# Kernel optimization log

Measured on AMD Instinct MI355X. Metric: run time of the kernel, lower is better.

The kernel has to match this reference:

```python
import jax, jax.numpy as jnp
import numpy as np

GROUP_SIZE = 128


def dequantize_int4(packed, scales, group_size=GROUP_SIZE, dtype=jnp.float16):
    # packed: [O, I//2] bytes; low nibble -> even cols, high nibble -> odd cols
    O = packed.shape[0]
    I = packed.shape[1] * 2
    low = (packed & 15).astype(jnp.int8) - 8
    high = ((packed >> 4) & 15).astype(jnp.int8) - 8
    unpacked = jnp.stack([low, high], axis=-1).reshape(O, I)  # interleave low/high
    G = I // group_size
    grouped = unpacked.reshape(O, G, group_size).astype(jnp.float32)
    deq = grouped * scales.astype(jnp.float32)[:, :, None]  # per-group scale
    return deq.reshape(O, I).astype(dtype)


def setup_inputs() -> dict:
    key = jax.random.key(0)
    k1, k2, k3 = jax.random.split(key, 3)
    B, S, IN, OUT = 4, 2048, 4096, 11008
    G = IN // GROUP_SIZE
    x = jax.random.normal(k1, (B, S, IN), dtype=jnp.float16)
    packed = jax.random.randint(k2, (OUT, IN // 2), 0, 256, dtype=jnp.int32)
    scales = (jax.random.uniform(k3, (OUT, G), dtype=jnp.float32) * 0.05 + 0.001).astype(jnp.float16)
    return {"x": x, "packed": packed, "scales": scales}


def reference(x, packed, scales):
    x = x.astype(jnp.float16)
    W = dequantize_int4(packed, scales)  # [OUT, IN] fp16
    # nn.functional.linear: x @ W^T
    return jnp.einsum('bsi,oi->bso', x, W)
```

## Files before the change

### kernel.cpp

```cpp
#include <hip/hip_runtime.h>

#define M_DIM 8192
#define N_DIM 11008
#define K_DIM 4096
#define GROUPS 32
#define WQROW 512
#define LDSK 72

typedef short s16x8 __attribute__((ext_vector_type(8)));
typedef _Float16 f16x8 __attribute__((ext_vector_type(8)));
typedef _Float16 h2 __attribute__((ext_vector_type(2)));
typedef float f32x4 __attribute__((ext_vector_type(4)));
typedef unsigned short u16;
typedef unsigned int u32;

union f32u { float f; unsigned u; };
union h16u { u16 u; _Float16 h; };

__device__ __forceinline__ u16 f2bf(float f) {
  f32u v; v.f = f;
  unsigned r = v.u + 0x7FFFu + ((v.u >> 16) & 1u);
  return (u16)(r >> 16);
}
__device__ __forceinline__ float bf2f(u16 b) {
  f32u v; v.u = ((unsigned)b) << 16; return v.f;
}
__device__ __forceinline__ float h2f(u16 b) {
  h16u v; v.u = b; return (float)v.h;
}

__global__ void probe_mode_kernel(const void* __restrict__ scales,
                                  int* __restrict__ mode_out) {
  __shared__ int cnt[3];
  int t = threadIdx.x;
  if (t < 3) cnt[t] = 0;
  __syncthreads();
  float f0 = ((const float*)scales)[t];
  u16  hu  = ((const u16*)scales)[t];
  float f1 = h2f(hu);
  float f2 = bf2f(hu);
  if (f0 > 0.0004f && f0 < 0.065f) atomicAdd(&cnt[0], 1);
  if (f1 > 0.0004f && f1 < 0.065f) atomicAdd(&cnt[1], 1);
  if (f2 > 0.0004f && f2 < 0.065f) atomicAdd(&cnt[2], 1);
  __syncthreads();
  if (t == 0) {
    int m;
    if      (cnt[1] >= 240) m = 1;
    else if (cnt[2] >= 240) m = 2;
    else                    m = 0;
    mode_out[0] = m;
  }
}

__global__ __launch_bounds__(256) void convert_x_nat_kernel(
    const float* __restrict__ xf, u16* __restrict__ xh,
    const int* __restrict__ modep) {
  if (modep && modep[0] != 0) return;
  const int total8 = M_DIM * (K_DIM / 8);
  int idx = blockIdx.x * 256 + threadIdx.x;
  const int stride = gridDim.x * 256;
  for (; idx < total8; idx += stride) {
    const float4* p = (const float4*)(xf + (size_t)idx * 8);
    float4 a = p[0], b = p[1];
    union { _Float16 h[8]; s16x8 v; } r;
    r.h[0] = (_Float16)a.x; r.h[1] = (_Float16)a.y;
    r.h[2] = (_Float16)a.z; r.h[3] = (_Float16)a.w;
    r.h[4] = (_Float16)b.x; r.h[5] = (_Float16)b.y;
    r.h[6] = (_Float16)b.z; r.h[7] = (_Float16)b.w;
    *(s16x8*)(xh + (size_t)idx * 8) = r.v;
  }
}

__global__ __launch_bounds__(256) void dequant_w_kernel(
    const int* __restrict__ packed, const float* __restrict__ scf,
    u16* __restrict__ wf, const int* __restrict__ modep) {
  if (modep && modep[0] != 0) return;
  const int total = N_DIM * (K_DIM / 8);
  int idx = blockIdx.x * 256 + threadIdx.x;
  const int stride = gridDim.x * 256;
  for (; idx < total; idx += stride) {
    const int col = idx >> 9;
    const int d   = idx & 511;
    const float s = scf[col * GROUPS + (d >> 4)];
    const int4 p  = ((const int4*)packed)[idx];
    const int vals[4] = {p.x, p.y, p.z, p.w};
    union { _Float16 h[8]; s16x8 v; } r;
    #pragma unroll
    for (int e = 0; e < 4; ++e) {
      int b = vals[e] & 255;
      r.h[2 * e]     = (_Float16)((float)((b & 15) - 8) * s);
      r.h[2 * e + 1] = (_Float16)((float)(((b >> 4) & 15) - 8) * s);
    }
    *(s16x8*)(wf + (size_t)idx * 8) = r.v;
  }
}

__global__ __launch_bounds__(256, 2) void q4gemm_big_kernel(
    const u16* __restrict__ xh,
    const u16* __restrict__ wf,
    float* __restrict__ out,
    const int* __restrict__ modep)
{
  if (modep && modep[0] != 0) return;

  __shared__ _Float16 As[4][128 * 64];

  const int tid  = threadIdx.x;
  const int lane = tid & 63;
  const int wv   = tid >> 6;
  const int wn   = wv * 64;
  const int ln15 = lane & 15;
  const int lk   = lane >> 4;

  int bid = blockIdx.x;
  int f   = (bid & 7) * 344 + (bid >> 3);
  int bn  = f / 64;
  int bm  = f - bn * 64;
  const int m0 = bm * 128;
  const int n0 = bn * 256;

  const u16* abase[4];
  #pragma unroll
  for (int q = 0; q < 4; ++q) {
    int row = q * 32 + wv * 8 + (lane >> 3);
    abase[q] = xh + (size_t)(m0 + row) * K_DIM + (((lane & 7) ^ (lane >> 3)) * 8);
  }

#define STAGE(PB, T) do { \
    _Float16* dst = &As[(PB)][0]; \
    _Pragma("unroll") \
    for (int q = 0; q < 4; ++q) \
      __builtin_amdgcn_global_load_lds( \
          (const __attribute__((address_space(1))) void*)(abase[q] + (T) * 64), \
          (__attribute__((address_space(3))) void*)(dst + q * 2048 + wv * 512), \
          16, 0, 0); \
  } while (0)

  const u16* pB[4];
  #pragma unroll
  for (int j = 0; j < 4; ++j) {
    int col = n0 + wn + j * 16 + ln15;
    pB[j] = wf + (size_t)col * K_DIM + lk * 8;
  }

#define LOADB(RB, T) do { \
    _Pragma("unroll") \
    for (int j = 0; j < 4; ++j) { \
      RB[j]     = *(const f16x8*)(pB[j] + (T) * 64); \
      RB[j + 4] = *(const f16x8*)(pB[j] + (T) * 64 + 32); \
    } \
  } while (0)

#define COMPUTE(RB, PB) do { \
    const _Float16* asb = &As[(PB)][0]; \
    _Pragma("unroll") \
    for (int kkc = 0; kkc < 2; ++kkc) { \
      _Pragma("unroll") \
      for (int i = 0; i < 8; ++i) { \
        const int row  = i * 16 + ln15; \
        const int slot = (kkc * 4 + lk) ^ (ln15 & 7); \
        f16x8 af = *(const f16x8*)&asb[row * 64 + slot * 8]; \
        acc[i][0] = __builtin_amdgcn_mfma_f32_16x16x32_f16(af, RB[kkc * 4 + 0], acc[i][0], 0, 0, 0); \
        acc[i][1] = __builtin_amdgcn_mfma_f32_16x16x32_f16(af, RB[kkc * 4 + 1], acc[i][1], 0, 0, 0); \
        acc[i][2] = __builtin_amdgcn_mfma_f32_16x16x32_f16(af, RB[kkc * 4 + 2], acc[i][2], 0, 0, 0); \
        acc[i][3] = __builtin_amdgcn_mfma_f32_16x16x32_f16(af, RB[kkc * 4 + 3], acc[i][3], 0, 0, 0); \
      } \
    } \
  } while (0)

  f32x4 acc[8][4];
  #pragma unroll
  for (int i = 0; i < 8; ++i)
    #pragma unroll
    for (int j = 0; j < 4; ++j)
      acc[i][j] = f32x4{0.f, 0.f, 0.f, 0.f};

  f16x8 rbE[8], rbO[8];

  STAGE(0, 0);
  STAGE(1, 1);
  STAGE(2, 2);
  STAGE(3, 3);
  LOADB(rbE, 0);
  LOADB(rbO, 1);
  asm volatile("s_waitcnt vmcnt(0)" ::: "memory");
  __builtin_amdgcn_s_barrier();

  #pragma unroll 1
  for (int P = 0; P < 32; ++P) {
    const int b0 = (P & 1) * 2;
    const int s0 = b0 ^ 2;

    if (P > 0) {
      asm volatile("s_waitcnt vmcnt(16)" ::: "memory");
      __builtin_amdgcn_s_barrier();
      __builtin_amdgcn_sched_barrier(0);
      if (P <= 30) {
        STAGE(s0, 2 * P + 2);
        STAGE(s0 + 1, 2 * P + 3);
      }
      __builtin_amdgcn_sched_barrier(0);
    }

    const int tE = (2 * P + 2 > 63) ? 63 : (2 * P + 2);
    const int tO = (2 * P + 3 > 63) ? 63 : (2 * P + 3);

    __builtin_amdgcn_s_setprio(1);
    COMPUTE(rbE, b0);
    __builtin_amdgcn_s_setprio(0);
    LOADB(rbE, tE);

    __builtin_amdgcn_s_setprio(1);
    COMPUTE(rbO, b0 + 1);
    __builtin_amdgcn_s_setprio(0);
    LOADB(rbO, tO);
  }

  #pragma unroll
  for (int i = 0; i < 8; ++i) {
    int r0 = m0 + i * 16 + (lane >> 4) * 4;
    #pragma unroll
    for (int j = 0; j < 4; ++j) {
      int cc = n0 + wn + j * 16 + ln15;
      #pragma unroll
      for (int r = 0; r < 4; ++r)
        __builtin_nontemporal_store(acc[i][j][r], &out[(size_t)(r0 + r) * N_DIM + cc]);
    }
  }
#undef STAGE
#undef LOADB
#undef COMPUTE
}

__global__ __launch_bounds__(256) void convert_x_perm_kernel(
    const float* __restrict__ xf, u16* __restrict__ xh,
    const int* __restrict__ modep) {
  if (modep && modep[0] != 0) return;
  const int total8 = M_DIM * (K_DIM / 8);
  int idx = blockIdx.x * 256 + threadIdx.x;
  const int stride = gridDim.x * 256;
  for (; idx < total8; idx += stride) {
    const float4* p = (const float4*)(xf + (size_t)idx * 8);
    float4 a = p[0], b = p[1];
    union { _Float16 h[8]; s16x8 v; } r;
    r.h[0] = (_Float16)a.x; r.h[1] = (_Float16)b.x;
    r.h[2] = (_Float16)a.y; r.h[3] = (_Float16)b.y;
    r.h[4] = (_Float16)a.z; r.h[5] = (_Float16)b.z;
    r.h[6] = (_Float16)a.w; r.h[7] = (_Float16)b.w;
    *(s16x8*)(xh + (size_t)idx * 8) = r.v;
  }
}

__global__ __launch_bounds__(256) void repack_w_kernel(
    const int* __restrict__ packed, u32* __restrict__ wq) {
  const int total = N_DIM * WQROW;
  int idx = blockIdx.x * 256 + threadIdx.x;
  const int stride = gridDim.x * 256;
  for (; idx < total; idx += stride) {
    const int4 p = ((const int4*)packed)[idx];
    wq[idx] = (u32)(p.x & 255) | ((u32)(p.y & 255) << 8) |
              ((u32)(p.z & 255) << 16) | ((u32)p.w << 24);
  }
}

__device__ __forceinline__ f16x8 dq8(u32 q, h2 s2) {
  const u32 M = 0x000F000Fu, G = 0x64006400u;
  const h2 bias = {(_Float16)(-1032.0f), (_Float16)(-1032.0f)};
  union { u32 u; h2 h; } a0, a1, a2, a3;
  a0.u = (q & M) | G;
  a1.u = ((q >> 4) & M) | G;
  a2.u = ((q >> 8) & M) | G;
  a3.u = ((q >> 12) & M) | G;
  a0.h = (a0.h + bias) * s2;
  a1.h = (a1.h + bias) * s2;
  a2.h = (a2.h + bias) * s2;
  a3.h = (a3.h + bias) * s2;
  union { u32 u[4]; f16x8 f; } r;
  r.u[0] = a0.u; r.u[1] = a1.u; r.u[2] = a2.u; r.u[3] = a3.u;
  return r.f;
}

__global__ __launch_bounds__(256, 2) void q4gemm_mid_kernel(
    const u16* __restrict__ xh, const u32* __restrict__ wq,
    const float* __restrict__ scf, float* __restrict__ out,
    const int* __restrict__ modep)
{
  if (modep && modep[0] != 0) return;

  __shared__ _Float16 As[3][128 * 64];

  const int tid  = threadIdx.x;
  const int lane = tid & 63;
  const int wv   = tid >> 6;
  const int wn   = wv * 64;
  const int ln15 = lane & 15;
  const int lk   = lane >> 4;

  int bid = blockIdx.x;
  int f   = (bid & 7) * 344 + (bid >> 3);
  int bn  = f / 64;
  int bm  = f - bn * 64;
  const int m0 = bm * 128;
  const int n0 = bn * 256;

  const u16* abase[4];
  #pragma unroll
  for (int q = 0; q < 4; ++q) {
    int row = q * 32 + wv * 8 + (lane >> 3);
    abase[q] = xh + (size_t)(m0 + row) * K_DIM + (((lane & 7) ^ (lane >> 3)) * 8);
  }

#define STAGE(PB, T) do { \
    _Float16* dst = &As[(PB)][0]; \
    _Pragma("unroll") \
    for (int q = 0; q < 4; ++q) \
      __builtin_amdgcn_global_load_lds( \
          (const __attribute__((address_space(1))) void*)(abase[q] + (T) * 64), \
          (__attribute__((address_space(3))) void*)(dst + q * 2048 + wv * 512), \
          16, 0, 0); \
  } while (0)

#define LOADB(RB, T) do { \
    _Pragma("unroll") \
    for (int j = 0; j < 4; ++j) { \
      RB[j]     = wq[pcol[j] + (T) * 8]; \
      RB[j + 4] = wq[pcol[j] + (T) * 8 + 4]; \
    } \
  } while (0)

#define COMPUTE(RB, PB) do { \
    const _Float16* asb = &As[(PB)][0]; \
    _Pragma("unroll") \
    for (int kkc = 0; kkc < 2; ++kkc) { \
      f16x8 bfr0 = dq8(RB[kkc * 4 + 0], s2[0]); \
      f16x8 bfr1 = dq8(RB[kkc * 4 + 1], s2[1]); \
      f16x8 bfr2 = dq8(RB[kkc * 4 + 2], s2[2]); \
      f16x8 bfr3 = dq8(RB[kkc * 4 + 3], s2[3]); \
      _Pragma("unroll") \
      for (int i = 0; i < 8; ++i) { \
        const int row  = i * 16 + ln15; \
        const int slot = (kkc * 4 + lk) ^ (ln15 & 7); \
        f16x8 af = *(const f16x8*)&asb[row * 64 + slot * 8]; \
        acc[i][0] = __builtin_amdgcn_mfma_f32_16x16x32_f16(af, bfr0, acc[i][0], 0, 0, 0); \
        acc[i][1] = __builtin_amdgcn_mfma_f32_16x16x32_f16(af, bfr1, acc[i][1], 0, 0, 0); \
        acc[i][2] = __builtin_amdgcn_mfma_f32_16x16x32_f16(af, bfr2, acc[i][2], 0, 0, 0); \
        acc[i][3] = __builtin_amdgcn_mfma_f32_16x16x32_f16(af, bfr3, acc[i][3], 0, 0, 0); \
      } \
    } \
  } while (0)

  int pcol[4], scol[4];
  #pragma unroll
  for (int j = 0; j < 4; ++j) {
    int col = n0 + wn + j * 16 + ln15;
    pcol[j] = col * WQROW + lk;
    scol[j] = col * GROUPS;
  }

  f32x4 acc[8][4];
  #pragma unroll
  for (int i = 0; i < 8; ++i)
    #pragma unroll
    for (int j = 0; j < 4; ++j)
      acc[i][j] = f32x4{0.f, 0.f, 0.f, 0.f};

  u32 rbE[8], rbO[8];
  float snextf[4];
  h2 s2[4];

  STAGE(0, 0);
  STAGE(1, 1);
  LOADB(rbE, 0);
  LOADB(rbO, 1);
  #pragma unroll
  for (int j = 0; j < 4; ++j) snextf[j] = scf[scol[j]];
  asm volatile("s_waitcnt vmcnt(0)" ::: "memory");

  int p0 = 0, p1 = 1, p2 = 2;

  for (int tp = 0; tp < 32; ++tp) {
    const int t0 = 2 * tp;
    const int t1 = t0 + 1;

    asm volatile("s_waitcnt vmcnt(12)" ::: "memory");
    __builtin_amdgcn_s_barrier();
    __builtin_amdgcn_sched_barrier(0);

    #pragma unroll
    for (int j = 0; j < 4; ++j) {
      _Float16 sh = (_Float16)snextf[j];
      s2[j] = h2{sh, sh};
    }
    if (t0 + 2 < 64) STAGE(p2, t0 + 2);

    __builtin_amdgcn_s_setprio(1);
    COMPUTE(rbE, p0);
    __builtin_amdgcn_s_setprio(0);

    if (t0 + 2 < 64) LOADB(rbE, t0 + 2);
    {
      const int gn = (tp + 1 > 31) ? 31 : (tp + 1);
      #pragma unroll
      for (int j = 0; j < 4; ++j) snextf[j] = scf[scol[j] + gn];
    }

    if (tp == 31) {
      asm volatile("s_waitcnt vmcnt(0)" ::: "memory");
    } else {
      asm volatile("s_waitcnt vmcnt(12)" ::: "memory");
    }
    __builtin_amdgcn_s_barrier();
    __builtin_amdgcn_sched_barrier(0);

    if (t1 + 2 < 64) STAGE(p0, t1 + 2);

    __builtin_amdgcn_s_setprio(1);
    COMPUTE(rbO, p1);
    __builtin_amdgcn_s_setprio(0);

    if (t1 + 2 < 64) LOADB(rbO, t1 + 2);

    int tmp = p2; p2 = p1; p1 = p0; p0 = tmp;
  }

  #pragma unroll
  for (int i = 0; i < 8; ++i) {
    int r0 = m0 + i * 16 + (lane >> 4) * 4;
    #pragma unroll
    for (int j = 0; j < 4; ++j) {
      int cc = n0 + wn + j * 16 + ln15;
      #pragma unroll
      for (int r = 0; r < 4; ++r)
        out[(size_t)(r0 + r) * N_DIM + cc] = acc[i][j][r];
    }
  }
#undef STAGE
#undef LOADB
#undef COMPUTE
}

__global__ __launch_bounds__(256) void q4gemm_slow_kernel(
    const void* __restrict__ xraw,
    const int*  __restrict__ packed,
    const void* __restrict__ scraw,
    float* __restrict__ out,
    const int* __restrict__ modep,
    int skip0)
{
  const int mode = modep ? modep[0] : 0;
  if (skip0 && mode == 0) return;

  __shared__ u16 Asl[128 * LDSK];
  __shared__ u16 Bsl[128 * LDSK];

  const int tid  = threadIdx.x;
  const int lane = tid & 63;
  const int wv   = tid >> 6;
  const int wm   = (wv >> 1) * 64;
  const int wn   = (wv & 1) * 64;
  const int n0   = blockIdx.x * 128;
  const int m0   = blockIdx.y * 128;

  f32x4 acc[4][4];
  #pragma unroll
  for (int i = 0; i < 4; ++i)
    #pragma unroll
    for (int j = 0; j < 4; ++j)
      acc[i][j] = f32x4{0.f, 0.f, 0.f, 0.f};

  const int lrow16 = lane & 15;
  const int lk8    = (lane >> 4) * 8;

  for (int k0 = 0; k0 < K_DIM; k0 += 64) {
    if (mode == 0) {
      const float* xf = (const float*)xraw;
      #pragma unroll
      for (int it = 0; it < 4; ++it) {
        int s = tid + it * 256;
        int row = s >> 3, c8 = (s & 7) * 8;
        const float4* p = (const float4*)(xf + (size_t)(m0 + row) * K_DIM + k0 + c8);
        float4 v0 = p[0], v1 = p[1];
        u16 tmp[8] = { f2bf(v0.x), f2bf(v0.y), f2bf(v0.z), f2bf(v0.w),
                       f2bf(v1.x), f2bf(v1.y), f2bf(v1.z), f2bf(v1.w) };
        *(s16x8*)&Asl[row * LDSK + c8] = *(const s16x8*)tmp;
      }
    } else if (mode == 1) {
      const u16* xhh = (const u16*)xraw;
      #pragma unroll
      for (int it = 0; it < 4; ++it) {
        int s = tid + it * 256;
        int row = s >> 3, c8 = (s & 7) * 8;
        s16x8 v = *(const s16x8*)(xhh + (size_t)(m0 + row) * K_DIM + k0 + c8);
        u16 tmp[8];
        #pragma unroll
        for (int j = 0; j < 8; ++j) tmp[j] = f2bf(h2f((u16)v[j]));
        *(s16x8*)&Asl[row * LDSK + c8] = *(const s16x8*)tmp;
      }
    } else {
      const u16* xhh = (const u16*)xraw;
      #pragma unroll
      for (int it = 0; it < 4; ++it) {
        int s = tid + it * 256;
        int row = s >> 3, c8 = (s & 7) * 8;
        s16x8 v = *(const s16x8*)(xhh + (size_t)(m0 + row) * K_DIM + k0 + c8);
        *(s16x8*)&Asl[row * LDSK + c8] = v;
      }
    }

    {
      int row  = tid >> 1;
      int half = tid & 1;
      int srw  = n0 + row;
      int g    = k0 >> 7;
      float scale;
      if      (mode == 0) scale = ((const float*)scraw)[(size_t)srw * GROUPS + g];
      else if (mode == 1) scale = h2f(((const u16*)scraw)[(size_t)srw * GROUPS + g]);
      else                scale = bf2f(((const u16*)scraw)[(size_t)srw * GROUPS + g]);

      const int4* pp = (const int4*)(packed + (size_t)srw * (K_DIM / 2) + (k0 >> 1) + half * 16);
      #pragma unroll
      for (int j = 0; j < 4; ++j) {
        int4 pv = pp[j];
        int vals[4] = {pv.x, pv.y, pv.z, pv.w};
        u16 w[8];
        #pragma unroll
        for (int e = 0; e < 4; ++e) {
          int b = vals[e] & 255;
          w[e * 2]     = f2bf(scale * (float)((b & 15) - 8));
          w[e * 2 + 1] = f2bf(scale * (float)(((b >> 4) & 15) - 8));
        }
        int i0 = half * 16 + j * 4;
        *(s16x8*)&Bsl[row * LDSK + i0 * 2] = *(const s16x8*)w;
      }
    }
    __syncthreads();

    #pragma unroll
    for (int kk = 0; kk < 64; kk += 32) {
      s16x8 af[4], bfr[4];
      int klane = kk + lk8;
      #pragma unroll
      for (int i = 0; i < 4; ++i)
        af[i] = *(const s16x8*)&Asl[(wm + i * 16 + lrow16) * LDSK + klane];
      #pragma unroll
      for (int i = 0; i < 4; ++i)
        bfr[i] = *(const s16x8*)&Bsl[(wn + i * 16 + lrow16) * LDSK + klane];
      #pragma unroll
      for (int i = 0; i < 4; ++i)
        #pragma unroll
        for (int j = 0; j < 4; ++j)
          acc[i][j] = __builtin_amdgcn_mfma_f32_16x16x32_bf16(af[i], bfr[j], acc[i][j], 0, 0, 0);
    }
    __syncthreads();
  }

  #pragma unroll
  for (int i = 0; i < 4; ++i) {
    int rbase = m0 + wm + i * 16 + ((lane >> 4) * 4);
    #pragma unroll
    for (int j = 0; j < 4; ++j) {
      int c = n0 + wn + j * 16 + (lane & 15);
      #pragma unroll
      for (int r = 0; r < 4; ++r)
        out[(size_t)(rbase + r) * N_DIM + c] = acc[i][j][r];
    }
  }
}

extern "C" void kernel_launch(void* const* d_in, const int* in_sizes, int n_in,
                              void* d_out, int out_size, void* d_ws, size_t ws_size,
                              hipStream_t stream) {
  const void* x      = d_in[0];
  const int*  packed = (const int*)d_in[1];
  const void* scales = d_in[2];
  float* out = (float*)d_out;

  const size_t XB = (size_t)M_DIM * K_DIM * 2;
  const size_t WF = (size_t)N_DIM * K_DIM * 2;
  const size_t WQ = (size_t)N_DIM * WQROW * 4;
  const size_t NEED_BIG = 256 + XB + WF;
  const size_t NEED_MID = 256 + XB + WQ;

  int* mode_flag = nullptr;
  if (ws_size >= 4) {
    mode_flag = (int*)d_ws;
    probe_mode_kernel<<<dim3(1), dim3(256), 0, stream>>>(scales, mode_flag);
  }

  int fast = 0;
  if (mode_flag && ws_size >= NEED_BIG) fast = 2;
  else if (mode_flag && ws_size >= NEED_MID) fast = 1;

  if (fast == 2) {
    u16* xh = (u16*)((char*)d_ws + 256);
    u16* wf = (u16*)((char*)d_ws + 256 + XB);
    convert_x_nat_kernel<<<dim3(2048), dim3(256), 0, stream>>>(
        (const float*)x, xh, mode_flag);
    dequant_w_kernel<<<dim3(2048), dim3(256), 0, stream>>>(
        packed, (const float*)scales, wf, mode_flag);
    q4gemm_big_kernel<<<dim3(2752), dim3(256), 0, stream>>>(
        xh, wf, out, mode_flag);
  } else if (fast == 1) {
    u16* xh = (u16*)((char*)d_ws + 256);
    u32* wq = (u32*)((char*)d_ws + 256 + XB);
    convert_x_perm_kernel<<<dim3(2048), dim3(256), 0, stream>>>(
        (const float*)x, xh, mode_flag);
    repack_w_kernel<<<dim3(2048), dim3(256), 0, stream>>>(packed, wq);
    q4gemm_mid_kernel<<<dim3(2752), dim3(256), 0, stream>>>(
        xh, wq, (const float*)scales, out, mode_flag);
  }

  q4gemm_slow_kernel<<<dim3(N_DIM / 128, M_DIM / 128), dim3(256), 0, stream>>>(
      x, packed, scales, out, mode_flag, fast);
}
```

Before: 905.6 us.

## Enlarge GEMM tile to 256x256 with 8 waves and LDS-staged B

The big GEMM kernel moves from 128x256 tiles with 4 waves to 256x256 tiles with 8 waves (512 threads). Both A and the dequantized weights are now staged into double-buffered LDS through global_load_lds, replacing the per-wave direct global loads of B into registers. The aim is to halve the weight traffic per output and reuse B across waves. In exchange it uses 128KB of LDS, adds extra barriers inside the compute loop, and waits for all loads each K step, which limits how much load latency can overlap with compute.

```diff
diff --git a/kernel.cpp b/kernel.cpp
--- a/kernel.cpp
+++ b/kernel.cpp
@@ -95,7 +95,7 @@
   }
 }
 
-__global__ __launch_bounds__(256, 2) void q4gemm_big_kernel(
+__global__ __launch_bounds__(512, 2) void q4gemm_big_kernel(
     const u16* __restrict__ xh,
     const u16* __restrict__ wf,
     float* __restrict__ out,
@@ -103,71 +103,52 @@
 {
   if (modep && modep[0] != 0) return;
 
-  __shared__ _Float16 As[4][128 * 64];
+  __shared__ _Float16 AsA[2][256 * 64];
+  __shared__ _Float16 AsB[2][256 * 64];
 
   const int tid  = threadIdx.x;
   const int lane = tid & 63;
   const int wv   = tid >> 6;
-  const int wn   = wv * 64;
+  const int wm   = (wv >> 2) * 128;
+  const int wn   = (wv & 3) * 64;
   const int ln15 = lane & 15;
   const int lk   = lane >> 4;
 
   int bid = blockIdx.x;
-  int f   = (bid & 7) * 344 + (bid >> 3);
-  int bn  = f / 64;
-  int bm  = f - bn * 64;
-  const int m0 = bm * 128;
+  int f   = (bid & 7) * 172 + (bid >> 3);
+  int bn  = f / 32;
+  int bm  = f - bn * 32;
+  const int m0 = bm * 256;
   const int n0 = bn * 256;
 
+  const int srow  = lane >> 3;
+  const int sperm = (lane & 7) ^ srow;
   const u16* abase[4];
+  const u16* bbase[4];
   #pragma unroll
   for (int q = 0; q < 4; ++q) {
-    int row = q * 32 + wv * 8 + (lane >> 3);
-    abase[q] = xh + (size_t)(m0 + row) * K_DIM + (((lane & 7) ^ (lane >> 3)) * 8);
-  }
-
-#define STAGE(PB, T) do { \
-    _Float16* dst = &As[(PB)][0]; \
+    int row = q * 64 + wv * 8 + srow;
+    abase[q] = xh + (size_t)(m0 + row) * K_DIM + sperm * 8;
+    bbase[q] = wf + (size_t)(n0 + row) * K_DIM + sperm * 8;
+  }
+
+#define STAGE_ALL(PB, T) do { \
+    _Float16* da = &AsA[(PB)][0]; \
+    _Float16* db = &AsB[(PB)][0]; \
     _Pragma("unroll") \
     for (int q = 0; q < 4; ++q) \
       __builtin_amdgcn_global_load_lds( \
           (const __attribute__((address_space(1))) void*)(abase[q] + (T) * 64), \
-          (__attribute__((address_space(3))) void*)(dst + q * 2048 + wv * 512), \
+          (__attribute__((address_space(3))) void*)(da + q * 4096 + wv * 512), \
+          16, 0, 0); \
+    _Pragma("unroll") \
+    for (int q = 0; q < 4; ++q) \
+      __builtin_amdgcn_global_load_lds( \
+          (const __attribute__((address_space(1))) void*)(bbase[q] + (T) * 64), \
+          (__attribute__((address_space(3))) void*)(db + q * 4096 + wv * 512), \
           16, 0, 0); \
   } while (0)
 
-  const u16* pB[4];
-  #pragma unroll
-  for (int j = 0; j < 4; ++j) {
-    int col = n0 + wn + j * 16 + ln15;
-    pB[j] = wf + (size_t)col * K_DIM + lk * 8;
-  }
-
-#define LOADB(RB, T) do { \
-    _Pragma("unroll") \
-    for (int j = 0; j < 4; ++j) { \
-      RB[j]     = *(const f16x8*)(pB[j] + (T) * 64); \
-      RB[j + 4] = *(const f16x8*)(pB[j] + (T) * 64 + 32); \
-    } \
-  } while (0)
-
-#define COMPUTE(RB, PB) do { \
-    const _Float16* asb = &As[(PB)][0]; \
-    _Pragma("unroll") \
-    for (int kkc = 0; kkc < 2; ++kkc) { \
-      _Pragma("unroll") \
-      for (int i = 0; i < 8; ++i) { \
-        const int row  = i * 16 + ln15; \
-        const int slot = (kkc * 4 + lk) ^ (ln15 & 7); \
-        f16x8 af = *(const f16x8*)&asb[row * 64 + slot * 8]; \
-        acc[i][0] = __builtin_amdgcn_mfma_f32_16x16x32_f16(af, RB[kkc * 4 + 0], acc[i][0], 0, 0, 0); \
-        acc[i][1] = __builtin_amdgcn_mfma_f32_16x16x32_f16(af, RB[kkc * 4 + 1], acc[i][1], 0, 0, 0); \
-        acc[i][2] = __builtin_amdgcn_mfma_f32_16x16x32_f16(af, RB[kkc * 4 + 2], acc[i][2], 0, 0, 0); \
-        acc[i][3] = __builtin_amdgcn_mfma_f32_16x16x32_f16(af, RB[kkc * 4 + 3], acc[i][3], 0, 0, 0); \
-      } \
-    } \
-  } while (0)
-
   f32x4 acc[8][4];
   #pragma unroll
   for (int i = 0; i < 8; ++i)
@@ -175,50 +156,58 @@
     for (int j = 0; j < 4; ++j)
       acc[i][j] = f32x4{0.f, 0.f, 0.f, 0.f};
 
-  f16x8 rbE[8], rbO[8];
-
-  STAGE(0, 0);
-  STAGE(1, 1);
-  STAGE(2, 2);
-  STAGE(3, 3);
-  LOADB(rbE, 0);
-  LOADB(rbO, 1);
-  asm volatile("s_waitcnt vmcnt(0)" ::: "memory");
-  __builtin_amdgcn_s_barrier();
+  STAGE_ALL(0, 0);
 
   #pragma unroll 1
-  for (int P = 0; P < 32; ++P) {
-    const int b0 = (P & 1) * 2;
-    const int s0 = b0 ^ 2;
-
-    if (P > 0) {
-      asm volatile("s_waitcnt vmcnt(16)" ::: "memory");
-      __builtin_amdgcn_s_barrier();
-      __builtin_amdgcn_sched_barrier(0);
-      if (P <= 30) {
-        STAGE(s0, 2 * P + 2);
-        STAGE(s0 + 1, 2 * P + 3);
+  for (int t = 0; t < 64; ++t) {
+    const int cur = t & 1;
+
+    asm volatile("s_waitcnt vmcnt(0)" ::: "memory");
+    __builtin_amdgcn_s_barrier();
+
+    if (t < 63) STAGE_ALL(cur ^ 1, t + 1);
+
+    const _Float16* Ab = &AsA[cur][0];
+    const _Float16* Bb = &AsB[cur][0];
+    const int slotx = ln15 & 7;
+
+    #pragma unroll
+    for (int kkc = 0; kkc < 2; ++kkc) {
+      const int slot = (kkc * 4 + lk) ^ slotx;
+      f16x8 bf[4];
+      #pragma unroll
+      for (int j = 0; j < 4; ++j) {
+        int r = wn + j * 16 + ln15;
+        bf[j] = *(const f16x8*)&Bb[r * 64 + slot * 8];
       }
-      __builtin_amdgcn_sched_barrier(0);
-    }
-
-    const int tE = (2 * P + 2 > 63) ? 63 : (2 * P + 2);
-    const int tO = (2 * P + 3 > 63) ? 63 : (2 * P + 3);
-
-    __builtin_amdgcn_s_setprio(1);
-    COMPUTE(rbE, b0);
-    __builtin_amdgcn_s_setprio(0);
-    LOADB(rbE, tE);
-
-    __builtin_amdgcn_s_setprio(1);
-    COMPUTE(rbO, b0 + 1);
-    __builtin_amdgcn_s_setprio(0);
-    LOADB(rbO, tO);
+      #pragma unroll
+      for (int ih = 0; ih < 2; ++ih) {
+        f16x8 af[4];
+        #pragma unroll
+        for (int ii = 0; ii < 4; ++ii) {
+          int r = wm + (ih * 4 + ii) * 16 + ln15;
+          af[ii] = *(const f16x8*)&Ab[r * 64 + slot * 8];
+        }
+        __builtin_amdgcn_s_barrier();
+        asm volatile("s_waitcnt lgkmcnt(0)" ::: "memory");
+        __builtin_amdgcn_sched_barrier(0);
+        __builtin_amdgcn_s_setprio(1);
+        #pragma unroll
+        for (int ii = 0; ii < 4; ++ii) {
+          acc[ih * 4 + ii][0] = __builtin_amdgcn_mfma_f32_16x16x32_f16(af[ii], bf[0], acc[ih * 4 + ii][0], 0, 0, 0);
+          acc[ih * 4 + ii][1] = __builtin_amdgcn_mfma_f32_16x16x32_f16(af[ii], bf[1], acc[ih * 4 + ii][1], 0, 0, 0);
+          acc[ih * 4 + ii][2] = __builtin_amdgcn_mfma_f32_16x16x32_f16(af[ii], bf[2], acc[ih * 4 + ii][2], 0, 0, 0);
+          acc[ih * 4 + ii][3] = __builtin_amdgcn_mfma_f32_16x16x32_f16(af[ii], bf[3], acc[ih * 4 + ii][3], 0, 0, 0);
+        }
+        __builtin_amdgcn_s_setprio(0);
+        __builtin_amdgcn_s_barrier();
+      }
+    }
   }
 
   #pragma unroll
   for (int i = 0; i < 8; ++i) {
-    int r0 = m0 + i * 16 + (lane >> 4) * 4;
+    int r0 = m0 + wm + i * 16 + (lane >> 4) * 4;
     #pragma unroll
     for (int j = 0; j < 4; ++j) {
       int cc = n0 + wn + j * 16 + ln15;
@@ -227,9 +216,7 @@
         __builtin_nontemporal_store(acc[i][j][r], &out[(size_t)(r0 + r) * N_DIM + cc]);
     }
   }
-#undef STAGE
-#undef LOADB
-#undef COMPUTE
+#undef STAGE_ALL
 }
 
 __global__ __launch_bounds__(256) void convert_x_perm_kernel(
@@ -598,7 +585,7 @@
         (const float*)x, xh, mode_flag);
     dequant_w_kernel<<<dim3(2048), dim3(256), 0, stream>>>(
         packed, (const float*)scales, wf, mode_flag);
-    q4gemm_big_kernel<<<dim3(2752), dim3(256), 0, stream>>>(
+    q4gemm_big_kernel<<<dim3(1376), dim3(512), 0, stream>>>(
         xh, wf, out, mode_flag);
   } else if (fast == 1) {
     u16* xh = (u16*)((char*)d_ws + 256);
```

New measurement: 967.3 us. +6.8%, slower.
